# Kernel tuning notes

Measured on AMD Instinct MI355X. Metric: run time of the kernel, lower is better.

The kernel has to match this reference:

```python
import jax, jax.numpy as jnp
import numpy as np
import math

NUM_HEADS = 8
WINDOW_SIZE = 1025
GLOBAL_TOKENS = 512  # effectively min(4, GLOBAL_TOKENS) indices are used, as in the torch code


def setup_inputs() -> dict:
    key = jax.random.key(0)
    k0, k1, k2 = jax.random.split(key, 3)
    B, C, H, W = 2, 256, 64, 64
    x = jax.random.normal(k0, (B, C, H, W), dtype=jnp.float32)
    # proj1: Linear(C, 3C); proj2: Linear(C, C). Stored as [in, out] matrices.
    w1 = jax.random.normal(k1, (C, 3 * C), dtype=jnp.float32) * 0.02
    b1 = jnp.zeros((3 * C,), dtype=jnp.float32)
    w2 = jax.random.normal(k2, (C, C), dtype=jnp.float32) * 0.02
    b2 = jnp.zeros((C,), dtype=jnp.float32)
    return {"x": x, "w1": w1, "b1": b1, "w2": w2, "b2": b2}


def _longformer_bias(L, W, window_size, global_tokens, dtype):
    # band: |i - j| <= window_size // 2  (matches start/end loop in torch code)
    i = jnp.arange(L)
    band = jnp.abs(i[:, None] - i[None, :]) <= (window_size // 2)
    gidx = [0, W - 1, L - W, L - 1][:global_tokens]
    g = jnp.zeros((L,), dtype=bool).at[jnp.array(gidx)].set(True)
    mask = band | g[:, None] | g[None, :]
    return jnp.where(mask, jnp.array(0.0, dtype), jnp.array(-jnp.inf, dtype))


def reference(x, w1, b1, w2, b2):
    B, C, H, W = x.shape
    L = H * W
    hd = C // NUM_HEADS
    # b c h w -> b (h w) c
    xt = x.reshape(B, C, L).transpose(0, 2, 1)
    qkv = xt @ w1 + b1  # [B, L, 3C]
    # 'b L (C H K)' with K=3, H=heads: last dim factors as (head_dim, heads, 3)
    qkv = qkv.reshape(B, L, hd, NUM_HEADS, 3).transpose(4, 0, 3, 1, 2)  # [3, B, Hh, L, hd]
    q, k, v = qkv[0], qkv[1], qkv[2]
    bias = _longformer_bias(L, W, WINDOW_SIZE, GLOBAL_TOKENS, x.dtype)
    scale = math.sqrt(hd)
    attn = jnp.einsum('bhqc,bhkc->bhqk', q, k) / scale + bias
    attn = jax.nn.softmax(attn, axis=-1)
    o = jnp.einsum('bhqk,bhkc->bhqc', attn, v)  # [B, Hh, L, hd]
    # 'b H (h w) C -> b h w (C H)': channel index = c*num_heads + head
    o = o.transpose(0, 2, 3, 1).reshape(B, H, W, hd * NUM_HEADS)
    out = o @ w2 + b2  # [B, H, W, C]
    return out.transpose(0, 3, 1, 2)  # b h w C -> b C h w
```

## Files before the change

kernel.cpp:

```cpp
#include <hip/hip_runtime.h>
#include <hip/hip_bf16.h>

#define BB 2
#define CC 256
#define HEADS 8
#define HD 32
#define LL 4096
#define HALF_WIN 512

using short8  = __attribute__((ext_vector_type(8))) short;
using short4v = __attribute__((ext_vector_type(4))) short;
using float4v = __attribute__((ext_vector_type(4))) float;

__device__ __forceinline__ ushort f2bf(float x) {
    uint u = __float_as_uint(x);
    u += 0x7fff + ((u >> 16) & 1);
    return (ushort)(u >> 16);
}
__device__ __forceinline__ float ubf(ushort u) {
    return __uint_as_float((uint)u << 16);
}
__device__ __forceinline__ uint pk2bf(float a, float b) {
#if __has_builtin(__builtin_amdgcn_cvt_pk_bf16_f32)
    typedef __bf16 v2bf __attribute__((ext_vector_type(2)));
    union { v2bf v; uint u; } cv;
    cv.v = __builtin_amdgcn_cvt_pk_bf16_f32(a, b);
    return cv.u;
#else
    return (uint)f2bf(a) | ((uint)f2bf(b) << 16);
#endif
}

#define QSCALE 0.25503485f

__global__ __launch_bounds__(256) void wt_kernel(const float* __restrict__ w1,
                                                 const float* __restrict__ w2,
                                                 ushort* __restrict__ w1t,
                                                 ushort* __restrict__ w2t) {
    __shared__ float tl[16][17];
    const int tx = threadIdx.x & 15, ty = threadIdx.x >> 4;
    const int ci0 = blockIdx.x * 16;
    const int y = blockIdx.y;
    if (y < 48) {
        int j0 = y * 16;
        tl[ty][tx] = w1[(size_t)(ci0 + ty) * 768 + j0 + tx];
        __syncthreads();
        w1t[(size_t)(j0 + ty) * CC + ci0 + tx] = f2bf(tl[tx][ty]);
    } else {
        int co0 = (y - 48) * 16;
        tl[ty][tx] = w2[(size_t)(ci0 + ty) * CC + co0 + tx];
        __syncthreads();
        w2t[(size_t)(co0 + ty) * CC + ci0 + tx] = f2bf(tl[tx][ty]);
    }
}

__global__ __launch_bounds__(256) void qkv_kernel(const float* __restrict__ x,
                                                  const ushort* __restrict__ w1t,
                                                  const float* __restrict__ b1,
                                                  ushort* __restrict__ qb,
                                                  ushort* __restrict__ kb,
                                                  ushort* __restrict__ vt) {
    __shared__ __align__(16) ushort xs[64 * 264];
    const int dg = blockIdx.x;
    const int l0 = blockIdx.y * 64;
    const int b  = blockIdx.z;
    const int t  = threadIdx.x;
    const int w  = t >> 6, ln = t & 63, c = ln & 15, g = ln >> 4;

    {
        const int l  = t & 63;
        const int cg = (t >> 6) * 4;
#pragma unroll
        for (int p = 0; p < 16; p++) {
            int c0 = p * 16 + cg;
            float a0 = x[((size_t)b * CC + c0 + 0) * LL + l0 + l];
            float a1 = x[((size_t)b * CC + c0 + 1) * LL + l0 + l];
            float a2 = x[((size_t)b * CC + c0 + 2) * LL + l0 + l];
            float a3 = x[((size_t)b * CC + c0 + 3) * LL + l0 + l];
            uint2 u;
            u.x = pk2bf(a0, a1);
            u.y = pk2bf(a2, a3);
            *(uint2*)&xs[l * 264 + c0] = u;
        }
    }
    __syncthreads();

    const int jbase = dg * 192 + w * 48;
    float4v acc[3][4] = {};
#pragma unroll
    for (int ks = 0; ks < 8; ks++) {
        short8 af[3], bfr[4];
#pragma unroll
        for (int jt = 0; jt < 3; jt++)
            af[jt] = *(const short8*)(w1t + (size_t)(jbase + jt * 16 + c) * CC + ks * 32 + g * 8);
#pragma unroll
        for (int lt = 0; lt < 4; lt++)
            bfr[lt] = *(const short8*)&xs[(lt * 16 + c) * 264 + ks * 32 + g * 8];
#pragma unroll
        for (int jt = 0; jt < 3; jt++)
#pragma unroll
            for (int lt = 0; lt < 4; lt++)
                acc[jt][lt] = __builtin_amdgcn_mfma_f32_16x16x32_bf16(af[jt], bfr[lt], acc[jt][lt], 0, 0, 0);
    }
    __syncthreads();

    ushort* qs  = xs;
    ushort* ksm = xs + 64 * 72;
    ushort* vs  = xs + 2 * 64 * 72;

#pragma unroll
    for (int jt = 0; jt < 3; jt++) {
#pragma unroll
        for (int r = 0; r < 4; r++) {
            int j = jbase + jt * 16 + g * 4 + r;
            float bias = b1[j];
            int t3 = j % 3, h = (j / 3) & 7, dl = (j / 24) & 7;
            int slot = h * 8 + dl;
            float v0 = acc[jt][0][r] + bias;
            float v1 = acc[jt][1][r] + bias;
            float v2 = acc[jt][2][r] + bias;
            float v3 = acc[jt][3][r] + bias;
            if (t3 == 0) { v0 *= QSCALE; v1 *= QSCALE; v2 *= QSCALE; v3 *= QSCALE; }
            uint u01 = pk2bf(v0, v1);
            uint u23 = pk2bf(v2, v3);
            ushort* dst = (t3 == 0) ? qs : (t3 == 1) ? ksm : vs;
            int stride = (t3 == 2) ? 74 : 72;
            dst[(0 * 16 + c) * stride + slot] = (ushort)u01;
            dst[(1 * 16 + c) * stride + slot] = (ushort)(u01 >> 16);
            dst[(2 * 16 + c) * stride + slot] = (ushort)u23;
            dst[(3 * 16 + c) * stride + slot] = (ushort)(u23 >> 16);
        }
    }
    __syncthreads();

    {
        const int l = t & 63;
#pragma unroll
        for (int p = 0; p < 2; p++) {
            int h = p * 4 + (t >> 6);
            size_t rowq = (((size_t)(b * 8 + h) * 4 + dg) * LL + l0 + l) * 8;
            *(short8*)(qb + rowq) = *(const short8*)&qs[l * 72 + h * 8];
            *(short8*)(kb + rowq) = *(const short8*)&ksm[l * 72 + h * 8];
        }
#pragma unroll
        for (int p = 0; p < 16; p++) {
            int hd = p * 4 + (t >> 6);
            vt[((size_t)(b * 8 + (hd >> 3)) * HD + dg * 8 + (hd & 7)) * LL + l0 + l] = vs[l * 74 + hd];
        }
    }
}

__device__ __forceinline__ int gcol_of(int tt) {
    return (tt == 0) ? 0 : (tt == 3) ? 63 : (tt == 252) ? LL - 64 : (tt == 255) ? LL - 1 : -1;
}

__global__ __launch_bounds__(256) void attn_kernel(const ushort* __restrict__ qb,
                                                   const ushort* __restrict__ kb,
                                                   const ushort* __restrict__ vt,
                                                   ushort* __restrict__ obuf) {
    __shared__ __align__(16) ushort pshare[4][576];
    const int n  = blockIdx.x;
    const int bh = ((n & 7) << 1) | ((n >> 3) & 1);
    const int it = n >> 4;
    const int i0 = it * 64;
    const int t  = threadIdx.x;
    const int w  = t >> 6;
    const int ln = t & 63;
    const int c  = ln & 15;
    const int g  = ln >> 4;

    const size_t slab = ((size_t)bh * 4 + g) * LL;
    const int i = i0 + w * 16 + c;

    const short8 qf = *(const short8*)(qb + (slab + i) * 8);

    float4v o0 = {0.f, 0.f, 0.f, 0.f}, o1 = {0.f, 0.f, 0.f, 0.f};
    float dsum = 0.f;

    int t0 = it * 4 - 32; if (t0 < 0) t0 = 0;
    int t1 = it * 4 + 35; if (t1 > 255) t1 = 255;
    int tf0 = it * 4 - 28; if (tf0 < 0) tf0 = 0;
    int tf1 = it * 4 + 31; if (tf1 > 255) tf1 = 255;

    int ml[12], nm = 0;
    for (int tt = t0; tt < tf0; tt++) ml[nm++] = tt;
    for (int tt = tf1 + 1; tt <= t1; tt++) ml[nm++] = tt;
    const int gt[4] = {0, 3, 252, 255};
#pragma unroll
    for (int e = 0; e < 4; e++)
        if (gt[e] < t0 || gt[e] > t1) ml[nm++] = gt[e];

    ushort* wb = &pshare[w][0];
    const ushort* vb = vt + (size_t)bh * HD * LL;

    const int npair_f = (tf1 - tf0 + 1) >> 1;
    const ushort* kp  = kb + (slab + (size_t)(tf0 * 16 + c)) * 8;
    const ushort* vp0 = vb + (size_t)c * LL + tf0 * 16 + g * 8;
    const ushort* vp1 = vp0 + 16 * LL;
    for (int m = 0; m < npair_f; m++) {
        const short8 kfA = *(const short8*)kp;
        const short8 kfB = *(const short8*)(kp + 128);
        kp += 256;
        float4v zero = {0.f, 0.f, 0.f, 0.f};
        float4v sA = __builtin_amdgcn_mfma_f32_16x16x32_bf16(kfA, qf, zero, 0, 0, 0);
        float4v sB = __builtin_amdgcn_mfma_f32_16x16x32_bf16(kfB, qf, zero, 0, 0, 0);

        float pA[4], pB[4];
#pragma unroll
        for (int r = 0; r < 4; r++) { pA[r] = exp2f(sA[r]); dsum += pA[r]; }
#pragma unroll
        for (int r = 0; r < 4; r++) { pB[r] = exp2f(sB[r]); dsum += pB[r]; }

        uint2 ua, ub2;
        ua.x  = pk2bf(pA[0], pA[1]);
        ua.y  = pk2bf(pA[2], pA[3]);
        ub2.x = pk2bf(pB[0], pB[1]);
        ub2.y = pk2bf(pB[2], pB[3]);
        *(uint2*)&wb[c * 36 + 4 * g]      = ua;
        *(uint2*)&wb[c * 36 + 16 + 4 * g] = ub2;

        union { short8 s8; short4v s4[2]; } pu;
        pu.s4[0] = *(const short4v*)&wb[c * 36 + 8 * g];
        pu.s4[1] = *(const short4v*)&wb[c * 36 + 8 * g + 4];
        const short8 pf = pu.s8;

        const short8 v0f = *(const short8*)vp0;
        const short8 v1f = *(const short8*)vp1;
        vp0 += 32; vp1 += 32;
        o0 = __builtin_amdgcn_mfma_f32_16x16x32_bf16(pf, v0f, o0, 0, 0, 0);
        o1 = __builtin_amdgcn_mfma_f32_16x16x32_bf16(pf, v1f, o1, 0, 0, 0);
    }

    for (int m = 0; m < nm; m += 2) {
        const int tA = ml[m], tB = ml[m + 1];
        const int gA = gcol_of(tA), gB = gcol_of(tB);
        const short8 kfA = *(const short8*)(kb + (slab + (size_t)(tA * 16 + c)) * 8);
        const short8 kfB = *(const short8*)(kb + (slab + (size_t)(tB * 16 + c)) * 8);
        float4v zero = {0.f, 0.f, 0.f, 0.f};
        float4v sA = __builtin_amdgcn_mfma_f32_16x16x32_bf16(kfA, qf, zero, 0, 0, 0);
        float4v sB = __builtin_amdgcn_mfma_f32_16x16x32_bf16(kfB, qf, zero, 0, 0, 0);

        float pA[4], pB[4];
#pragma unroll
        for (int r = 0; r < 4; r++) {
            int j = tA * 16 + g * 4 + r;
            bool ok = ((unsigned)(i - j + HALF_WIN) <= 2u * HALF_WIN) | (j == gA);
            pA[r] = ok ? exp2f(sA[r]) : 0.f;
            dsum += pA[r];
        }
#pragma unroll
        for (int r = 0; r < 4; r++) {
            int j = tB * 16 + g * 4 + r;
            bool ok = ((unsigned)(i - j + HALF_WIN) <= 2u * HALF_WIN) | (j == gB);
            pB[r] = ok ? exp2f(sB[r]) : 0.f;
            dsum += pB[r];
        }

        uint2 ua, ub2;
        ua.x  = pk2bf(pA[0], pA[1]);
        ua.y  = pk2bf(pA[2], pA[3]);
        ub2.x = pk2bf(pB[0], pB[1]);
        ub2.y = pk2bf(pB[2], pB[3]);
        *(uint2*)&wb[c * 36 + 4 * g]      = ua;
        *(uint2*)&wb[c * 36 + 16 + 4 * g] = ub2;

        union { short8 s8; short4v s4[2]; } pu;
        pu.s4[0] = *(const short4v*)&wb[c * 36 + 8 * g];
        pu.s4[1] = *(const short4v*)&wb[c * 36 + 8 * g + 4];
        const short8 pf = pu.s8;

        const int jv = (g < 2) ? tA * 16 + g * 8 : tB * 16 + (g - 2) * 8;
        const short8 v0f = *(const short8*)(vb + (size_t)c * LL + jv);
        const short8 v1f = *(const short8*)(vb + (size_t)(16 + c) * LL + jv);
        o0 = __builtin_amdgcn_mfma_f32_16x16x32_bf16(pf, v0f, o0, 0, 0, 0);
        o1 = __builtin_amdgcn_mfma_f32_16x16x32_bf16(pf, v1f, o1, 0, 0, 0);
    }

    dsum += __shfl_xor(dsum, 16);
    dsum += __shfl_xor(dsum, 32);

    const int b = bh >> 3, hh = bh & 7;
#pragma unroll
    for (int r = 0; r < 4; r++) {
        float dn = __shfl(dsum, g * 4 + r);
        float inv = 1.0f / dn;
        int irow = i0 + w * 16 + g * 4 + r;
        size_t rowb = ((size_t)b * LL + irow) * CC;
        obuf[rowb + (size_t)c * 8 + hh]        = f2bf(o0[r] * inv);
        obuf[rowb + (size_t)(16 + c) * 8 + hh] = f2bf(o1[r] * inv);
    }
}

__global__ __launch_bounds__(256) void attn_global_partial(const ushort* __restrict__ qb,
                                                           const ushort* __restrict__ kb,
                                                           const ushort* __restrict__ vt,
                                                           float* __restrict__ gpart) {
    __shared__ float qs[4][32];
    __shared__ float sc[4][256];
    const int ch = blockIdx.x;
    const int bh = blockIdx.y;
    const int t  = threadIdx.x;
    const int gidx[4] = {0, 63, LL - 64, LL - 1};

    if (t < 128) {
        int r = t >> 5, dd = t & 31;
        int i = gidx[r];
        qs[r][dd] = ubf(qb[(((size_t)bh * 4 + (dd >> 3)) * LL + i) * 8 + (dd & 7)]);
    }
    __syncthreads();

    const int j = ch * 256 + t;
    float dot[4] = {};
#pragma unroll
    for (int s = 0; s < 4; s++) {
        const short8 kf = *(const short8*)(kb + (((size_t)bh * 4 + s) * LL + j) * 8);
#pragma unroll
        for (int e = 0; e < 8; e++) {
            float kv = ubf((ushort)kf[e]);
#pragma unroll
            for (int r = 0; r < 4; r++) dot[r] += qs[r][s * 8 + e] * kv;
        }
    }
#pragma unroll
    for (int r = 0; r < 4; r++) sc[r][t] = exp2f(dot[r]);
    __syncthreads();

    const int w = t >> 6, ln = t & 63;
    float den = sc[w][ln] + sc[w][ln + 64] + sc[w][ln + 128] + sc[w][ln + 192];
#pragma unroll
    for (int o = 1; o < 64; o <<= 1) den += __shfl_xor(den, o);

    const int dd = ln & 31, half = ln >> 5;
    float acc = 0.f;
    const ushort* vrow = vt + ((size_t)bh * HD + dd) * LL + ch * 256 + half * 128;
#pragma unroll
    for (int q8 = 0; q8 < 16; q8++) {
        const short8 v8 = *(const short8*)(vrow + q8 * 8);
#pragma unroll
        for (int e = 0; e < 8; e++) acc += sc[w][half * 128 + q8 * 8 + e] * ubf((ushort)v8[e]);
    }
    acc += __shfl_xor(acc, 32);

    float* gp = gpart + (((size_t)bh * 16 + ch) * 4 + w) * 33;
    if (ln < 32) gp[dd] = acc;
    if (ln == 0) gp[32] = den;
}

__global__ __launch_bounds__(128) void attn_global_combine(const float* __restrict__ gpart,
                                                           ushort* __restrict__ obuf) {
    const int bh = blockIdx.x;
    const int t  = threadIdx.x;
    const int r  = t >> 5, dd = t & 31;
    const int gidx[4] = {0, 63, LL - 64, LL - 1};
    float pv = 0.f, den = 0.f;
#pragma unroll
    for (int ch = 0; ch < 16; ch++) {
        const float* gp = gpart + (((size_t)bh * 16 + ch) * 4 + r) * 33;
        pv  += gp[dd];
        den += gp[32];
    }
    const int b = bh >> 3, hh = bh & 7, i = gidx[r];
    obuf[((size_t)b * LL + i) * CC + dd * 8 + hh] = f2bf(pv / den);
}

__global__ __launch_bounds__(256) void proj_kernel(const ushort* __restrict__ obuf,
                                                   const ushort* __restrict__ w2t,
                                                   const float* __restrict__ b2,
                                                   float* __restrict__ out) {
    const int co0 = blockIdx.x * 16;
    const int l0  = blockIdx.y * 256 + (threadIdx.x >> 6) * 64;
    const int b   = blockIdx.z;
    const int ln  = threadIdx.x & 63;
    const int c   = ln & 15, g = ln >> 4;

    float4v acc[4] = {};
    const ushort* arow = w2t + (size_t)(co0 + c) * CC + g * 8;
    const ushort* brow = obuf + ((size_t)b * LL + l0 + c) * CC + g * 8;
#pragma unroll
    for (int ks = 0; ks < 8; ks++) {
        const short8 af = *(const short8*)(arow + ks * 32);
#pragma unroll
        for (int nf = 0; nf < 4; nf++) {
            const short8 bf = *(const short8*)(brow + (size_t)nf * 16 * CC + ks * 32);
            acc[nf] = __builtin_amdgcn_mfma_f32_16x16x32_bf16(af, bf, acc[nf], 0, 0, 0);
        }
    }
#pragma unroll
    for (int nf = 0; nf < 4; nf++) {
#pragma unroll
        for (int r = 0; r < 4; r++) {
            int co = co0 + g * 4 + r;
            int l  = l0 + nf * 16 + c;
            out[((size_t)b * CC + co) * LL + l] = acc[nf][r] + b2[co];
        }
    }
}

extern "C" void kernel_launch(void* const* d_in, const int* in_sizes, int n_in,
                              void* d_out, int out_size, void* d_ws, size_t ws_size,
                              hipStream_t stream) {
    const float* x  = (const float*)d_in[0];
    const float* w1 = (const float*)d_in[1];
    const float* b1 = (const float*)d_in[2];
    const float* w2 = (const float*)d_in[3];
    const float* b2 = (const float*)d_in[4];
    float* out = (float*)d_out;

    const size_t QKE = (size_t)BB * HEADS * LL * HD;
    const size_t OBE = (size_t)BB * LL * CC;
    ushort* qb  = (ushort*)d_ws;
    ushort* kb  = qb + QKE;
    ushort* vt  = kb + QKE;
    ushort* ob  = vt + QKE;
    float*  gp  = (float*)(ob + OBE);
    ushort* w2t = (ushort*)(gp + 16 * 16 * 4 * 33);
    ushort* w1t = w2t + CC * CC;

    wt_kernel<<<dim3(16, 64), 256, 0, stream>>>(w1, w2, w1t, w2t);
    qkv_kernel<<<dim3(4, 64, 2), 256, 0, stream>>>(x, w1t, b1, qb, kb, vt);
    attn_kernel<<<dim3(1024), 256, 0, stream>>>(qb, kb, vt, ob);
    attn_global_partial<<<dim3(16, 16), 256, 0, stream>>>(qb, kb, vt, gp);
    attn_global_combine<<<dim3(16), 128, 0, stream>>>(gp, ob);
    proj_kernel<<<dim3(16, 16, 2), 256, 0, stream>>>(ob, w2t, b2, out);
}
```

Measured before the change: 144.8 us.

## Split attention key range across two wave groups per block with LDS reduction

Doubles the attention block to 512 threads, so two sets of four waves each process half of the full-band key tiles for the same 64 query rows. The second set also handles the edge and global tiles, then writes its partial accumulators and row sums to shared memory. After a barrier the first set adds them in and finishes the output. The aim is more waves in flight and a shorter serial loop per wave, so memory and MFMA latency is better hidden. The cost is a barrier, an LDS partial-sum exchange, and possible load imbalance because one half also does the masked tiles.

```diff
diff --git a/kernel.cpp b/kernel.cpp
--- a/kernel.cpp
+++ b/kernel.cpp
@@ -154,23 +154,26 @@
     return (tt == 0) ? 0 : (tt == 3) ? 63 : (tt == 252) ? LL - 64 : (tt == 255) ? LL - 1 : -1;
 }
 
-__global__ __launch_bounds__(256) void attn_kernel(const ushort* __restrict__ qb,
+__global__ __launch_bounds__(512) void attn_kernel(const ushort* __restrict__ qb,
                                                    const ushort* __restrict__ kb,
                                                    const ushort* __restrict__ vt,
                                                    ushort* __restrict__ obuf) {
-    __shared__ __align__(16) ushort pshare[4][576];
+    __shared__ __align__(16) ushort pshare[8][576];
+    __shared__ float cbuf[4][64][9];
     const int n  = blockIdx.x;
     const int bh = ((n & 7) << 1) | ((n >> 3) & 1);
     const int it = n >> 4;
     const int i0 = it * 64;
     const int t  = threadIdx.x;
-    const int w  = t >> 6;
+    const int w8 = t >> 6;
+    const int wg = w8 & 3;
+    const int jh = w8 >> 2;
     const int ln = t & 63;
     const int c  = ln & 15;
     const int g  = ln >> 4;
 
     const size_t slab = ((size_t)bh * 4 + g) * LL;
-    const int i = i0 + w * 16 + c;
+    const int i = i0 + wg * 16 + c;
 
     const short8 qf = *(const short8*)(qb + (slab + i) * 8);
 
@@ -190,14 +193,18 @@
     for (int e = 0; e < 4; e++)
         if (gt[e] < t0 || gt[e] > t1) ml[nm++] = gt[e];
 
-    ushort* wb = &pshare[w][0];
+    ushort* wb = &pshare[w8][0];
     const ushort* vb = vt + (size_t)bh * HD * LL;
 
     const int npair_f = (tf1 - tf0 + 1) >> 1;
-    const ushort* kp  = kb + (slab + (size_t)(tf0 * 16 + c)) * 8;
-    const ushort* vp0 = vb + (size_t)c * LL + tf0 * 16 + g * 8;
+    const int h = npair_f >> 1;
+    const int mstart = jh ? h : 0;
+    const int mend   = jh ? npair_f : h;
+    const int tfs = tf0 + 2 * mstart;
+    const ushort* kp  = kb + (slab + (size_t)(tfs * 16 + c)) * 8;
+    const ushort* vp0 = vb + (size_t)c * LL + tfs * 16 + g * 8;
     const ushort* vp1 = vp0 + 16 * LL;
-    for (int m = 0; m < npair_f; m++) {
+    for (int m = mstart; m < mend; m++) {
         const short8 kfA = *(const short8*)kp;
         const short8 kfB = *(const short8*)(kp + 128);
         kp += 256;
@@ -231,49 +238,64 @@
         o1 = __builtin_amdgcn_mfma_f32_16x16x32_bf16(pf, v1f, o1, 0, 0, 0);
     }
 
-    for (int m = 0; m < nm; m += 2) {
-        const int tA = ml[m], tB = ml[m + 1];
-        const int gA = gcol_of(tA), gB = gcol_of(tB);
-        const short8 kfA = *(const short8*)(kb + (slab + (size_t)(tA * 16 + c)) * 8);
-        const short8 kfB = *(const short8*)(kb + (slab + (size_t)(tB * 16 + c)) * 8);
-        float4v zero = {0.f, 0.f, 0.f, 0.f};
-        float4v sA = __builtin_amdgcn_mfma_f32_16x16x32_bf16(kfA, qf, zero, 0, 0, 0);
-        float4v sB = __builtin_amdgcn_mfma_f32_16x16x32_bf16(kfB, qf, zero, 0, 0, 0);
-
-        float pA[4], pB[4];
-#pragma unroll
-        for (int r = 0; r < 4; r++) {
-            int j = tA * 16 + g * 4 + r;
-            bool ok = ((unsigned)(i - j + HALF_WIN) <= 2u * HALF_WIN) | (j == gA);
-            pA[r] = ok ? exp2f(sA[r]) : 0.f;
-            dsum += pA[r];
-        }
-#pragma unroll
-        for (int r = 0; r < 4; r++) {
-            int j = tB * 16 + g * 4 + r;
-            bool ok = ((unsigned)(i - j + HALF_WIN) <= 2u * HALF_WIN) | (j == gB);
-            pB[r] = ok ? exp2f(sB[r]) : 0.f;
-            dsum += pB[r];
-        }
-
-        uint2 ua, ub2;
-        ua.x  = pk2bf(pA[0], pA[1]);
-        ua.y  = pk2bf(pA[2], pA[3]);
-        ub2.x = pk2bf(pB[0], pB[1]);
-        ub2.y = pk2bf(pB[2], pB[3]);
-        *(uint2*)&wb[c * 36 + 4 * g]      = ua;
-        *(uint2*)&wb[c * 36 + 16 + 4 * g] = ub2;
-
-        union { short8 s8; short4v s4[2]; } pu;
-        pu.s4[0] = *(const short4v*)&wb[c * 36 + 8 * g];
-        pu.s4[1] = *(const short4v*)&wb[c * 36 + 8 * g + 4];
-        const short8 pf = pu.s8;
-
-        const int jv = (g < 2) ? tA * 16 + g * 8 : tB * 16 + (g - 2) * 8;
-        const short8 v0f = *(const short8*)(vb + (size_t)c * LL + jv);
-        const short8 v1f = *(const short8*)(vb + (size_t)(16 + c) * LL + jv);
-        o0 = __builtin_amdgcn_mfma_f32_16x16x32_bf16(pf, v0f, o0, 0, 0, 0);
-        o1 = __builtin_amdgcn_mfma_f32_16x16x32_bf16(pf, v1f, o1, 0, 0, 0);
+    if (jh == 1) {
+        for (int m = 0; m < nm; m += 2) {
+            const int tA = ml[m], tB = ml[m + 1];
+            const int gA = gcol_of(tA), gB = gcol_of(tB);
+            const short8 kfA = *(const short8*)(kb + (slab + (size_t)(tA * 16 + c)) * 8);
+            const short8 kfB = *(const short8*)(kb + (slab + (size_t)(tB * 16 + c)) * 8);
+            float4v zero = {0.f, 0.f, 0.f, 0.f};
+            float4v sA = __builtin_amdgcn_mfma_f32_16x16x32_bf16(kfA, qf, zero, 0, 0, 0);
+            float4v sB = __builtin_amdgcn_mfma_f32_16x16x32_bf16(kfB, qf, zero, 0, 0, 0);
+
+            float pA[4], pB[4];
+#pragma unroll
+            for (int r = 0; r < 4; r++) {
+                int j = tA * 16 + g * 4 + r;
+                bool ok = ((unsigned)(i - j + HALF_WIN) <= 2u * HALF_WIN) | (j == gA);
+                pA[r] = ok ? exp2f(sA[r]) : 0.f;
+                dsum += pA[r];
+            }
+#pragma unroll
+            for (int r = 0; r < 4; r++) {
+                int j = tB * 16 + g * 4 + r;
+                bool ok = ((unsigned)(i - j + HALF_WIN) <= 2u * HALF_WIN) | (j == gB);
+                pB[r] = ok ? exp2f(sB[r]) : 0.f;
+                dsum += pB[r];
+            }
+
+            uint2 ua, ub2;
+            ua.x  = pk2bf(pA[0], pA[1]);
+            ua.y  = pk2bf(pA[2], pA[3]);
+            ub2.x = pk2bf(pB[0], pB[1]);
+            ub2.y = pk2bf(pB[2], pB[3]);
+            *(uint2*)&wb[c * 36 + 4 * g]      = ua;
+            *(uint2*)&wb[c * 36 + 16 + 4 * g] = ub2;
+
+            union { short8 s8; short4v s4[2]; } pu;
+            pu.s4[0] = *(const short4v*)&wb[c * 36 + 8 * g];
+            pu.s4[1] = *(const short4v*)&wb[c * 36 + 8 * g + 4];
+            const short8 pf = pu.s8;
+
+            const int jv = (g < 2) ? tA * 16 + g * 8 : tB * 16 + (g - 2) * 8;
+            const short8 v0f = *(const short8*)(vb + (size_t)c * LL + jv);
+            const short8 v1f = *(const short8*)(vb + (size_t)(16 + c) * LL + jv);
+            o0 = __builtin_amdgcn_mfma_f32_16x16x32_bf16(pf, v0f, o0, 0, 0, 0);
+            o1 = __builtin_amdgcn_mfma_f32_16x16x32_bf16(pf, v1f, o1, 0, 0, 0);
+        }
+        float* cb = &cbuf[wg][ln][0];
+#pragma unroll
+        for (int r = 0; r < 4; r++) { cb[r] = o0[r]; cb[4 + r] = o1[r]; }
+        cb[8] = dsum;
+    }
+    __syncthreads();
+    if (jh == 1) return;
+
+    {
+        const float* cb = &cbuf[wg][ln][0];
+#pragma unroll
+        for (int r = 0; r < 4; r++) { o0[r] += cb[r]; o1[r] += cb[4 + r]; }
+        dsum += cb[8];
     }
 
     dsum += __shfl_xor(dsum, 16);
@@ -284,7 +306,7 @@
     for (int r = 0; r < 4; r++) {
         float dn = __shfl(dsum, g * 4 + r);
         float inv = 1.0f / dn;
-        int irow = i0 + w * 16 + g * 4 + r;
+        int irow = i0 + wg * 16 + g * 4 + r;
         size_t rowb = ((size_t)b * LL + irow) * CC;
         obuf[rowb + (size_t)c * 8 + hh]        = f2bf(o0[r] * inv);
         obuf[rowb + (size_t)(16 + c) * 8 + hh] = f2bf(o1[r] * inv);
@@ -418,7 +440,7 @@
 
     wt_kernel<<<dim3(16, 64), 256, 0, stream>>>(w1, w2, w1t, w2t);
     qkv_kernel<<<dim3(4, 64, 2), 256, 0, stream>>>(x, w1t, b1, qb, kb, vt);
-    attn_kernel<<<dim3(1024), 256, 0, stream>>>(qb, kb, vt, ob);
+    attn_kernel<<<dim3(1024), 512, 0, stream>>>(qb, kb, vt, ob);
     attn_global_partial<<<dim3(16, 16), 256, 0, stream>>>(qb, kb, vt, gp);
     attn_global_combine<<<dim3(16), 128, 0, stream>>>(gp, ob);
     proj_kernel<<<dim3(16, 16, 2), 256, 0, stream>>>(ob, w2t, b2, out);
```

After: 147.0 us. No clear change (+1.5%).

## Replace LDS P-transpose with cross-lane shuffles and use native exp2

Applied to the files above, without the earlier changes.

In the attention kernel, the shared-memory round trip that turned the exponentiated score fragment into the MFMA operand layout is removed. The fragment is now rearranged with eight cross-lane shuffles, and the PV MFMA operands are swapped so the output comes out transposed. That transposed output lets each lane normalize with its own row sum, with no per-row shuffle at the end. exp2f is also replaced by the hardware exp2 builtin, which skips range handling. The trade is eight shuffle ops per iteration instead of LDS stores and loads, plus a changed output store pattern.

```diff
diff --git a/kernel.cpp b/kernel.cpp
--- a/kernel.cpp
+++ b/kernel.cpp
@@ -28,6 +28,13 @@
     return cv.u;
 #else
     return (uint)f2bf(a) | ((uint)f2bf(b) << 16);
+#endif
+}
+__device__ __forceinline__ float rexp2(float x) {
+#if __has_builtin(__builtin_amdgcn_exp2f)
+    return __builtin_amdgcn_exp2f(x);
+#else
+    return exp2f(x);
 #endif
 }
 
@@ -154,11 +161,30 @@
     return (tt == 0) ? 0 : (tt == 3) ? 63 : (tt == 252) ? LL - 64 : (tt == 255) ? LL - 1 : -1;
 }
 
+__device__ __forceinline__ short8 ptrans(uint2 ua, uint2 ub, int c, int g) {
+    const int laneL = c + ((g & 1) << 5);
+    const int laneH = laneL + 16;
+    int a0 = __shfl((int)ua.x, laneL);
+    int a1 = __shfl((int)ua.y, laneL);
+    int a2 = __shfl((int)ua.x, laneH);
+    int a3 = __shfl((int)ua.y, laneH);
+    int b0 = __shfl((int)ub.x, laneL);
+    int b1 = __shfl((int)ub.y, laneL);
+    int b2 = __shfl((int)ub.x, laneH);
+    int b3 = __shfl((int)ub.y, laneH);
+    union { uint u[4]; short8 s8; } pf;
+    bool lo = (g < 2);
+    pf.u[0] = lo ? (uint)a0 : (uint)b0;
+    pf.u[1] = lo ? (uint)a1 : (uint)b1;
+    pf.u[2] = lo ? (uint)a2 : (uint)b2;
+    pf.u[3] = lo ? (uint)a3 : (uint)b3;
+    return pf.s8;
+}
+
 __global__ __launch_bounds__(256) void attn_kernel(const ushort* __restrict__ qb,
                                                    const ushort* __restrict__ kb,
                                                    const ushort* __restrict__ vt,
                                                    ushort* __restrict__ obuf) {
-    __shared__ __align__(16) ushort pshare[4][576];
     const int n  = blockIdx.x;
     const int bh = ((n & 7) << 1) | ((n >> 3) & 1);
     const int it = n >> 4;
@@ -190,7 +216,6 @@
     for (int e = 0; e < 4; e++)
         if (gt[e] < t0 || gt[e] > t1) ml[nm++] = gt[e];
 
-    ushort* wb = &pshare[w][0];
     const ushort* vb = vt + (size_t)bh * HD * LL;
 
     const int npair_f = (tf1 - tf0 + 1) >> 1;
@@ -207,28 +232,22 @@
 
         float pA[4], pB[4];
 #pragma unroll
-        for (int r = 0; r < 4; r++) { pA[r] = exp2f(sA[r]); dsum += pA[r]; }
-#pragma unroll
-        for (int r = 0; r < 4; r++) { pB[r] = exp2f(sB[r]); dsum += pB[r]; }
+        for (int r = 0; r < 4; r++) { pA[r] = rexp2(sA[r]); dsum += pA[r]; }
+#pragma unroll
+        for (int r = 0; r < 4; r++) { pB[r] = rexp2(sB[r]); dsum += pB[r]; }
 
         uint2 ua, ub2;
         ua.x  = pk2bf(pA[0], pA[1]);
         ua.y  = pk2bf(pA[2], pA[3]);
         ub2.x = pk2bf(pB[0], pB[1]);
         ub2.y = pk2bf(pB[2], pB[3]);
-        *(uint2*)&wb[c * 36 + 4 * g]      = ua;
-        *(uint2*)&wb[c * 36 + 16 + 4 * g] = ub2;
-
-        union { short8 s8; short4v s4[2]; } pu;
-        pu.s4[0] = *(const short4v*)&wb[c * 36 + 8 * g];
-        pu.s4[1] = *(const short4v*)&wb[c * 36 + 8 * g + 4];
-        const short8 pf = pu.s8;
+        const short8 pf = ptrans(ua, ub2, c, g);
 
         const short8 v0f = *(const short8*)vp0;
         const short8 v1f = *(const short8*)vp1;
         vp0 += 32; vp1 += 32;
-        o0 = __builtin_amdgcn_mfma_f32_16x16x32_bf16(pf, v0f, o0, 0, 0, 0);
-        o1 = __builtin_amdgcn_mfma_f32_16x16x32_bf16(pf, v1f, o1, 0, 0, 0);
+        o0 = __builtin_amdgcn_mfma_f32_16x16x32_bf16(v0f, pf, o0, 0, 0, 0);
+        o1 = __builtin_amdgcn_mfma_f32_16x16x32_bf16(v1f, pf, o1, 0, 0, 0);
     }
 
     for (int m = 0; m < nm; m += 2) {
@@ -245,14 +264,14 @@
         for (int r = 0; r < 4; r++) {
             int j = tA * 16 + g * 4 + r;
             bool ok = ((unsigned)(i - j + HALF_WIN) <= 2u * HALF_WIN) | (j == gA);
-            pA[r] = ok ? exp2f(sA[r]) : 0.f;
+            pA[r] = ok ? rexp2(sA[r]) : 0.f;
             dsum += pA[r];
         }
 #pragma unroll
         for (int r = 0; r < 4; r++) {
             int j = tB * 16 + g * 4 + r;
             bool ok = ((unsigned)(i - j + HALF_WIN) <= 2u * HALF_WIN) | (j == gB);
-            pB[r] = ok ? exp2f(sB[r]) : 0.f;
+            pB[r] = ok ? rexp2(sB[r]) : 0.f;
             dsum += pB[r];
         }
 
@@ -261,33 +280,25 @@
         ua.y  = pk2bf(pA[2], pA[3]);
         ub2.x = pk2bf(pB[0], pB[1]);
         ub2.y = pk2bf(pB[2], pB[3]);
-        *(uint2*)&wb[c * 36 + 4 * g]      = ua;
-        *(uint2*)&wb[c * 36 + 16 + 4 * g] = ub2;
-
-        union { short8 s8; short4v s4[2]; } pu;
-        pu.s4[0] = *(const short4v*)&wb[c * 36 + 8 * g];
-        pu.s4[1] = *(const short4v*)&wb[c * 36 + 8 * g + 4];
-        const short8 pf = pu.s8;
+        const short8 pf = ptrans(ua, ub2, c, g);
 
         const int jv = (g < 2) ? tA * 16 + g * 8 : tB * 16 + (g - 2) * 8;
         const short8 v0f = *(const short8*)(vb + (size_t)c * LL + jv);
         const short8 v1f = *(const short8*)(vb + (size_t)(16 + c) * LL + jv);
-        o0 = __builtin_amdgcn_mfma_f32_16x16x32_bf16(pf, v0f, o0, 0, 0, 0);
-        o1 = __builtin_amdgcn_mfma_f32_16x16x32_bf16(pf, v1f, o1, 0, 0, 0);
+        o0 = __builtin_amdgcn_mfma_f32_16x16x32_bf16(v0f, pf, o0, 0, 0, 0);
+        o1 = __builtin_amdgcn_mfma_f32_16x16x32_bf16(v1f, pf, o1, 0, 0, 0);
     }
 
     dsum += __shfl_xor(dsum, 16);
     dsum += __shfl_xor(dsum, 32);
+    const float inv = 1.0f / dsum;
 
     const int b = bh >> 3, hh = bh & 7;
+    const size_t rowb = ((size_t)b * LL + i0 + w * 16 + c) * CC;
 #pragma unroll
     for (int r = 0; r < 4; r++) {
-        float dn = __shfl(dsum, g * 4 + r);
-        float inv = 1.0f / dn;
-        int irow = i0 + w * 16 + g * 4 + r;
-        size_t rowb = ((size_t)b * LL + irow) * CC;
-        obuf[rowb + (size_t)c * 8 + hh]        = f2bf(o0[r] * inv);
-        obuf[rowb + (size_t)(16 + c) * 8 + hh] = f2bf(o1[r] * inv);
+        obuf[rowb + (size_t)(g * 4 + r) * 8 + hh]        = f2bf(o0[r] * inv);
+        obuf[rowb + (size_t)(16 + g * 4 + r) * 8 + hh]   = f2bf(o1[r] * inv);
     }
 }
 
@@ -322,7 +333,7 @@
         }
     }
 #pragma unroll
-    for (int r = 0; r < 4; r++) sc[r][t] = exp2f(dot[r]);
+    for (int r = 0; r < 4; r++) sc[r][t] = rexp2(dot[r]);
     __syncthreads();
 
     const int w = t >> 6, ln = t & 63;
```

Result: slower. 149.1 us (+3.0%).

## Split key range across warps with all query tiles per warp, reduce via LDS

Applied to the files above, without the earlier changes.

Each warp now holds all four 16-row query tiles and processes a quarter of the key pairs, so every K and V fragment load is reused across four query tiles instead of being reloaded by each warp. Partial O accumulators and row sums are exchanged through shared memory and summed at the end. The change also switches to the raw hardware exp2 builtin and adds a launch-bounds occupancy hint. In exchange it raises register pressure (16 accumulators), uses more LDS, and adds a final cross-warp reduction with a barrier.

```diff
diff --git a/kernel.cpp b/kernel.cpp
--- a/kernel.cpp
+++ b/kernel.cpp
@@ -28,6 +28,13 @@
     return cv.u;
 #else
     return (uint)f2bf(a) | ((uint)f2bf(b) << 16);
+#endif
+}
+__device__ __forceinline__ float rexp2(float x) {
+#if __has_builtin(__builtin_amdgcn_exp2f)
+    return __builtin_amdgcn_exp2f(x);
+#else
+    return exp2f(x);
 #endif
 }
 
@@ -154,11 +161,12 @@
     return (tt == 0) ? 0 : (tt == 3) ? 63 : (tt == 252) ? LL - 64 : (tt == 255) ? LL - 1 : -1;
 }
 
-__global__ __launch_bounds__(256) void attn_kernel(const ushort* __restrict__ qb,
-                                                   const ushort* __restrict__ kb,
-                                                   const ushort* __restrict__ vt,
-                                                   ushort* __restrict__ obuf) {
-    __shared__ __align__(16) ushort pshare[4][576];
+__global__ __launch_bounds__(256, 4) void attn_kernel(const ushort* __restrict__ qb,
+                                                      const ushort* __restrict__ kb,
+                                                      const ushort* __restrict__ vt,
+                                                      ushort* __restrict__ obuf) {
+    __shared__ __align__(16) ushort pshare[4][4][576];
+    __shared__ float cbuf[4][3][64][9];
     const int n  = blockIdx.x;
     const int bh = ((n & 7) << 1) | ((n >> 3) & 1);
     const int it = n >> 4;
@@ -170,12 +178,19 @@
     const int g  = ln >> 4;
 
     const size_t slab = ((size_t)bh * 4 + g) * LL;
-    const int i = i0 + w * 16 + c;
-
-    const short8 qf = *(const short8*)(qb + (slab + i) * 8);
-
-    float4v o0 = {0.f, 0.f, 0.f, 0.f}, o1 = {0.f, 0.f, 0.f, 0.f};
-    float dsum = 0.f;
+
+    short8 qf[4];
+#pragma unroll
+    for (int s = 0; s < 4; s++)
+        qf[s] = *(const short8*)(qb + (slab + i0 + s * 16 + c) * 8);
+
+    float4v o0[4], o1[4];
+#pragma unroll
+    for (int s = 0; s < 4; s++) {
+#pragma unroll
+        for (int r = 0; r < 4; r++) { o0[s][r] = 0.f; o1[s][r] = 0.f; }
+    }
+    float dsum[4] = {0.f, 0.f, 0.f, 0.f};
 
     int t0 = it * 4 - 32; if (t0 < 0) t0 = 0;
     int t1 = it * 4 + 35; if (t1 > 255) t1 = 255;
@@ -190,104 +205,137 @@
     for (int e = 0; e < 4; e++)
         if (gt[e] < t0 || gt[e] > t1) ml[nm++] = gt[e];
 
-    ushort* wb = &pshare[w][0];
     const ushort* vb = vt + (size_t)bh * HD * LL;
+    ushort* wbb = &pshare[w][0][0];
 
     const int npair_f = (tf1 - tf0 + 1) >> 1;
-    const ushort* kp  = kb + (slab + (size_t)(tf0 * 16 + c)) * 8;
-    const ushort* vp0 = vb + (size_t)c * LL + tf0 * 16 + g * 8;
+    const int qq = npair_f >> 2, rem = npair_f & 3;
+    const int mstart = w * qq + (w < rem ? w : rem);
+    const int mcount = qq + (w < rem ? 1 : 0);
+    const int tfs = tf0 + 2 * mstart;
+
+    const ushort* kp  = kb + (slab + (size_t)(tfs * 16 + c)) * 8;
+    const ushort* vp0 = vb + (size_t)c * LL + tfs * 16 + g * 8;
     const ushort* vp1 = vp0 + 16 * LL;
-    for (int m = 0; m < npair_f; m++) {
+    for (int m = 0; m < mcount; m++) {
         const short8 kfA = *(const short8*)kp;
         const short8 kfB = *(const short8*)(kp + 128);
         kp += 256;
-        float4v zero = {0.f, 0.f, 0.f, 0.f};
-        float4v sA = __builtin_amdgcn_mfma_f32_16x16x32_bf16(kfA, qf, zero, 0, 0, 0);
-        float4v sB = __builtin_amdgcn_mfma_f32_16x16x32_bf16(kfB, qf, zero, 0, 0, 0);
-
-        float pA[4], pB[4];
-#pragma unroll
-        for (int r = 0; r < 4; r++) { pA[r] = exp2f(sA[r]); dsum += pA[r]; }
-#pragma unroll
-        for (int r = 0; r < 4; r++) { pB[r] = exp2f(sB[r]); dsum += pB[r]; }
-
-        uint2 ua, ub2;
-        ua.x  = pk2bf(pA[0], pA[1]);
-        ua.y  = pk2bf(pA[2], pA[3]);
-        ub2.x = pk2bf(pB[0], pB[1]);
-        ub2.y = pk2bf(pB[2], pB[3]);
-        *(uint2*)&wb[c * 36 + 4 * g]      = ua;
-        *(uint2*)&wb[c * 36 + 16 + 4 * g] = ub2;
-
-        union { short8 s8; short4v s4[2]; } pu;
-        pu.s4[0] = *(const short4v*)&wb[c * 36 + 8 * g];
-        pu.s4[1] = *(const short4v*)&wb[c * 36 + 8 * g + 4];
-        const short8 pf = pu.s8;
-
         const short8 v0f = *(const short8*)vp0;
         const short8 v1f = *(const short8*)vp1;
         vp0 += 32; vp1 += 32;
-        o0 = __builtin_amdgcn_mfma_f32_16x16x32_bf16(pf, v0f, o0, 0, 0, 0);
-        o1 = __builtin_amdgcn_mfma_f32_16x16x32_bf16(pf, v1f, o1, 0, 0, 0);
-    }
-
-    for (int m = 0; m < nm; m += 2) {
-        const int tA = ml[m], tB = ml[m + 1];
+        float4v zero = {0.f, 0.f, 0.f, 0.f};
+#pragma unroll
+        for (int s = 0; s < 4; s++) {
+            float4v sA = __builtin_amdgcn_mfma_f32_16x16x32_bf16(kfA, qf[s], zero, 0, 0, 0);
+            float4v sB = __builtin_amdgcn_mfma_f32_16x16x32_bf16(kfB, qf[s], zero, 0, 0, 0);
+            float pA[4], pB[4];
+#pragma unroll
+            for (int r = 0; r < 4; r++) { pA[r] = rexp2(sA[r]); dsum[s] += pA[r]; }
+#pragma unroll
+            for (int r = 0; r < 4; r++) { pB[r] = rexp2(sB[r]); dsum[s] += pB[r]; }
+            uint2 ua, ub2;
+            ua.x  = pk2bf(pA[0], pA[1]);
+            ua.y  = pk2bf(pA[2], pA[3]);
+            ub2.x = pk2bf(pB[0], pB[1]);
+            ub2.y = pk2bf(pB[2], pB[3]);
+            ushort* wb = wbb + s * 576;
+            *(uint2*)&wb[c * 36 + 4 * g]      = ua;
+            *(uint2*)&wb[c * 36 + 16 + 4 * g] = ub2;
+        }
+#pragma unroll
+        for (int s = 0; s < 4; s++) {
+            const ushort* wb = wbb + s * 576;
+            union { short8 s8; short4v s4[2]; } pu;
+            pu.s4[0] = *(const short4v*)&wb[c * 36 + 8 * g];
+            pu.s4[1] = *(const short4v*)&wb[c * 36 + 8 * g + 4];
+            o0[s] = __builtin_amdgcn_mfma_f32_16x16x32_bf16(pu.s8, v0f, o0[s], 0, 0, 0);
+            o1[s] = __builtin_amdgcn_mfma_f32_16x16x32_bf16(pu.s8, v1f, o1[s], 0, 0, 0);
+        }
+    }
+
+    for (int p = 0; p < (nm >> 1); p++) {
+        if ((p & 3) != w) continue;
+        const int tA = ml[2 * p], tB = ml[2 * p + 1];
         const int gA = gcol_of(tA), gB = gcol_of(tB);
         const short8 kfA = *(const short8*)(kb + (slab + (size_t)(tA * 16 + c)) * 8);
         const short8 kfB = *(const short8*)(kb + (slab + (size_t)(tB * 16 + c)) * 8);
-        float4v zero = {0.f, 0.f, 0.f, 0.f};
-        float4v sA = __builtin_amdgcn_mfma_f32_16x16x32_bf16(kfA, qf, zero, 0, 0, 0);
-        float4v sB = __builtin_amdgcn_mfma_f32_16x16x32_bf16(kfB, qf, zero, 0, 0, 0);
-
-        float pA[4], pB[4];
-#pragma unroll
-        for (int r = 0; r < 4; r++) {
-            int j = tA * 16 + g * 4 + r;
-            bool ok = ((unsigned)(i - j + HALF_WIN) <= 2u * HALF_WIN) | (j == gA);
-            pA[r] = ok ? exp2f(sA[r]) : 0.f;
-            dsum += pA[r];
-        }
-#pragma unroll
-        for (int r = 0; r < 4; r++) {
-            int j = tB * 16 + g * 4 + r;
-            bool ok = ((unsigned)(i - j + HALF_WIN) <= 2u * HALF_WIN) | (j == gB);
-            pB[r] = ok ? exp2f(sB[r]) : 0.f;
-            dsum += pB[r];
-        }
-
-        uint2 ua, ub2;
-        ua.x  = pk2bf(pA[0], pA[1]);
-        ua.y  = pk2bf(pA[2], pA[3]);
-        ub2.x = pk2bf(pB[0], pB[1]);
-        ub2.y = pk2bf(pB[2], pB[3]);
-        *(uint2*)&wb[c * 36 + 4 * g]      = ua;
-        *(uint2*)&wb[c * 36 + 16 + 4 * g] = ub2;
-
-        union { short8 s8; short4v s4[2]; } pu;
-        pu.s4[0] = *(const short4v*)&wb[c * 36 + 8 * g];
-        pu.s4[1] = *(const short4v*)&wb[c * 36 + 8 * g + 4];
-        const short8 pf = pu.s8;
-
         const int jv = (g < 2) ? tA * 16 + g * 8 : tB * 16 + (g - 2) * 8;
         const short8 v0f = *(const short8*)(vb + (size_t)c * LL + jv);
         const short8 v1f = *(const short8*)(vb + (size_t)(16 + c) * LL + jv);
-        o0 = __builtin_amdgcn_mfma_f32_16x16x32_bf16(pf, v0f, o0, 0, 0, 0);
-        o1 = __builtin_amdgcn_mfma_f32_16x16x32_bf16(pf, v1f, o1, 0, 0, 0);
-    }
-
-    dsum += __shfl_xor(dsum, 16);
-    dsum += __shfl_xor(dsum, 32);
+        float4v zero = {0.f, 0.f, 0.f, 0.f};
+#pragma unroll
+        for (int s = 0; s < 4; s++) {
+            const int i = i0 + s * 16 + c;
+            float4v sA = __builtin_amdgcn_mfma_f32_16x16x32_bf16(kfA, qf[s], zero, 0, 0, 0);
+            float4v sB = __builtin_amdgcn_mfma_f32_16x16x32_bf16(kfB, qf[s], zero, 0, 0, 0);
+            float pA[4], pB[4];
+#pragma unroll
+            for (int r = 0; r < 4; r++) {
+                int j = tA * 16 + g * 4 + r;
+                bool ok = ((unsigned)(i - j + HALF_WIN) <= 2u * HALF_WIN) | (j == gA);
+                pA[r] = ok ? rexp2(sA[r]) : 0.f;
+                dsum[s] += pA[r];
+            }
+#pragma unroll
+            for (int r = 0; r < 4; r++) {
+                int j = tB * 16 + g * 4 + r;
+                bool ok = ((unsigned)(i - j + HALF_WIN) <= 2u * HALF_WIN) | (j == gB);
+                pB[r] = ok ? rexp2(sB[r]) : 0.f;
+                dsum[s] += pB[r];
+            }
+            uint2 ua, ub2;
+            ua.x  = pk2bf(pA[0], pA[1]);
+            ua.y  = pk2bf(pA[2], pA[3]);
+            ub2.x = pk2bf(pB[0], pB[1]);
+            ub2.y = pk2bf(pB[2], pB[3]);
+            ushort* wb = wbb + s * 576;
+            *(uint2*)&wb[c * 36 + 4 * g]      = ua;
+            *(uint2*)&wb[c * 36 + 16 + 4 * g] = ub2;
+        }
+#pragma unroll
+        for (int s = 0; s < 4; s++) {
+            const ushort* wb = wbb + s * 576;
+            union { short8 s8; short4v s4[2]; } pu;
+            pu.s4[0] = *(const short4v*)&wb[c * 36 + 8 * g];
+            pu.s4[1] = *(const short4v*)&wb[c * 36 + 8 * g + 4];
+            o0[s] = __builtin_amdgcn_mfma_f32_16x16x32_bf16(pu.s8, v0f, o0[s], 0, 0, 0);
+            o1[s] = __builtin_amdgcn_mfma_f32_16x16x32_bf16(pu.s8, v1f, o1[s], 0, 0, 0);
+        }
+    }
+
+#pragma unroll
+    for (int s = 0; s < 4; s++) {
+        if (s == w) continue;
+        float* cb = &cbuf[s][(w < s) ? w : w - 1][ln][0];
+#pragma unroll
+        for (int r = 0; r < 4; r++) { cb[r] = o0[s][r]; cb[4 + r] = o1[s][r]; }
+        cb[8] = dsum[s];
+    }
+    __syncthreads();
+
+    float4v O0 = o0[w], O1 = o1[w];
+    float ds = dsum[w];
+#pragma unroll
+    for (int k = 0; k < 3; k++) {
+        const float* cb = &cbuf[w][k][ln][0];
+#pragma unroll
+        for (int r = 0; r < 4; r++) { O0[r] += cb[r]; O1[r] += cb[4 + r]; }
+        ds += cb[8];
+    }
+
+    ds += __shfl_xor(ds, 16);
+    ds += __shfl_xor(ds, 32);
 
     const int b = bh >> 3, hh = bh & 7;
 #pragma unroll
     for (int r = 0; r < 4; r++) {
-        float dn = __shfl(dsum, g * 4 + r);
+        float dn = __shfl(ds, g * 4 + r);
         float inv = 1.0f / dn;
         int irow = i0 + w * 16 + g * 4 + r;
         size_t rowb = ((size_t)b * LL + irow) * CC;
-        obuf[rowb + (size_t)c * 8 + hh]        = f2bf(o0[r] * inv);
-        obuf[rowb + (size_t)(16 + c) * 8 + hh] = f2bf(o1[r] * inv);
+        obuf[rowb + (size_t)c * 8 + hh]        = f2bf(O0[r] * inv);
+        obuf[rowb + (size_t)(16 + c) * 8 + hh] = f2bf(O1[r] * inv);
     }
 }
 
@@ -322,7 +370,7 @@
         }
     }
 #pragma unroll
-    for (int r = 0; r < 4; r++) sc[r][t] = exp2f(dot[r]);
+    for (int r = 0; r < 4; r++) sc[r][t] = rexp2(dot[r]);
     __syncthreads();
 
     const int w = t >> 6, ln = t & 63;
```

Result: faster. 136.6 us (-5.6%).
